# Optimization experiments

Hardware: AMD Instinct MI355X
Metric: run time of the kernel (lower is better)

The kernel has to match this reference:

```python
import math
import jax, jax.numpy as jnp
import numpy as np

# hyperparameters (module defaults; w_scale overridden to 1.0)
EMA_SPEED = 0.05
REW_SENS = 1.0
LR = 0.0033
MOMENTUM = 0.4
UNTANH = 0.6
SPEED = 0.5
WIDTH = 0.1
WD = 0.01
LAT_DECAY = 0.01
NOISE_SCALE = 0.8
C_MOMENT = 0.99
W_SCALE = 1.0


def rms_norm(x, axis=-1):
    return x * jax.lax.rsqrt(jnp.mean(x * x, axis=axis, keepdims=True) + 1e-6)


def setup_inputs() -> dict:
    key = jax.random.key(0)
    ks = jax.random.split(key, 16)
    B, N, D = 16, 128, 64
    s = 1.0 / math.sqrt(D)
    return {
        'eye_env': jax.random.normal(ks[0], (B, D), jnp.float32),
        'stomach_env': jax.random.normal(ks[1], (B, D), jnp.float32),
        'state': jax.random.normal(ks[2], (B, N, D), jnp.float32),
        'output': jax.random.normal(ks[3], (B, N, D), jnp.float32),
        'W1': jax.random.normal(ks[4], (B, N, D, D), jnp.float32) * s,
        'W2': jax.random.normal(ks[5], (B, N, D, D), jnp.float32) * s,
        'W3': jax.random.normal(ks[6], (B, N, D, D), jnp.float32) * s,
        'M1': jax.random.normal(ks[7], (B, N, D, D), jnp.float32) * 0.2,
        'M2': jax.random.normal(ks[8], (B, N, D, D), jnp.float32) * 0.2,
        'M3': jax.random.normal(ks[9], (B, N, D, D), jnp.float32) * 0.2,
        'E_baseline': jax.random.uniform(ks[10], (B, N, D), jnp.float32),
        'A': jax.nn.softmax(jax.random.normal(ks[11], (B, N, N), jnp.float32), axis=2),
        'noise_A': jax.random.normal(ks[12], (B, N, N), jnp.float32),
        'noise1_raw': jax.random.normal(ks[13], (B, N, D), jnp.float32),
        'noise2_raw': jax.random.normal(ks[14], (B, N, D), jnp.float32),
        'step_counter': 0,
    }


def reference(eye_env, stomach_env, state, output, W1, W2, W3, M1, M2, M3,
              E_baseline, A, noise_A, noise1_raw, noise2_raw, step_counter):
    B, N, D = state.shape
    sc = jnp.float32(step_counter) + 1.0  # self.step_counter += 1

    # attention routing
    q = jnp.einsum('bnj,bnjk->bnk', state, W3)
    k = jnp.einsum('bnj,bnjk->bnk', state, W2)
    raw_A = jnp.einsum('bnd,bmd->bnm', q, k) / math.sqrt(D) + noise_A * 1e-5
    P_dense = jax.nn.softmax(raw_A, axis=2)
    keep = (P_dense > 1.0 / (N + 1.0)) | (P_dense == jnp.max(P_dense, axis=2, keepdims=True))
    P = jax.nn.softmax(jnp.where(keep, raw_A, -jnp.inf), axis=2)
    A_new = A * C_MOMENT + P * (1.0 - C_MOMENT)
    A_new = A_new.at[:, 0:2, :].set(0.0)

    # message passing + sensory clamp
    target = jnp.einsum('bnm,bmd->bnd', A_new, output)
    target = target.at[:, 0].set(eye_env).at[:, 1].set(stomach_env)

    # prediction
    raw_pred = jnp.einsum('bnj,bnjk->bnk', state, W1)
    raw = raw_pred - jnp.tanh(raw_pred) * UNTANH
    prediction = jnp.tanh(raw) * math.sqrt(2.0 + math.sqrt(2.0))

    err = prediction - target
    E_curr = jax.nn.softmax(err, axis=-1)
    bmask = (E_baseline == 0).astype(jnp.float32)
    Eb = E_baseline * (1.0 - bmask) + E_curr * bmask
    Eb = Eb * (1.0 - EMA_SPEED) + EMA_SPEED * E_curr
    advantage = E_curr - Eb
    R = -rms_norm(advantage[..., None] * REW_SENS)  # (B,N,D,1)
    mask = (Eb > 0).astype(jnp.float32)[..., None]

    # noise injection
    state_mag = jnp.sum(jnp.abs(state), axis=(-2, -1), keepdims=True)
    noise1 = noise1_raw / (1.0 + state_mag)
    noise2 = noise2_raw * jnp.std(err, ddof=1) * NOISE_SCALE
    noisy_state = state + noise1 + noise2

    # Hebbian outer-product gradient, G_NORM=1.0 -> rms-normalized
    lg = -jnp.einsum('bni,bnj->bnij', err, noisy_state)
    lg = rms_norm(lg, axis=(2, 3))

    plasticity = 1.0 - R
    grad1 = plasticity * lg * mask + LAT_DECAY * W3 - WD * W1
    grad2 = plasticity * lg * mask + LAT_DECAY * W1 - WD * W2
    grad3 = plasticity * lg * mask + LAT_DECAY * W2 - WD * W3

    # travelling gaussian column mask
    idx = jnp.arange(D, dtype=jnp.float32).reshape(1, 1, 1, D)
    center = (sc * SPEED) % D
    diff = jnp.abs(idx - center)
    diff = jnp.minimum(diff, D - diff)
    g_mask = jnp.exp(-diff ** 2 / (2.0 * WIDTH ** 2 + 1e-6))

    M1n = M1 * MOMENTUM + (1.0 - MOMENTUM) * (grad1 * g_mask)
    M2n = M2 * MOMENTUM + (1.0 - MOMENTUM) * (grad2 * g_mask)
    M3n = M3 * MOMENTUM + (1.0 - MOMENTUM) * (grad3 * g_mask)
    W1n = rms_norm(W1 + LR * M1n) * W_SCALE
    W2n = rms_norm(W2 + LR * M2n) * W_SCALE
    W3n = rms_norm(W3 + LR * M3n) * W_SCALE

    # new output = prediction, new state = target
    return prediction, target, A_new, W1n, W2n, W3n
```

## Files before the change

### kernel.cpp

```cpp
#include <hip/hip_runtime.h>
#include <hip/hip_bf16.h>

typedef __hip_bfloat16 bf16;
typedef float f32x4 __attribute__((ext_vector_type(4)));

__device__ __forceinline__ float b2f(bf16 x) { return __bfloat162float(x); }

template<bool F32>
__device__ __forceinline__ float ld(const void* p, size_t i) {
  if constexpr (F32) return ((const float*)p)[i];
  else return b2f(((const bf16*)p)[i]);
}

template<bool F32>
__device__ __forceinline__ void ld4(const void* p, size_t i, float v[4]) {
  if constexpr (F32) {
    const float4 a = *(const float4*)((const float*)p + i);
    v[0]=a.x; v[1]=a.y; v[2]=a.z; v[3]=a.w;
  } else {
    union { uint2 u; bf16 h[4]; } t;
    t.u = *(const uint2*)((const bf16*)p + i);
    #pragma unroll
    for (int c = 0; c < 4; ++c) v[c] = b2f(t.h[c]);
  }
}

template<bool F32>
__device__ __forceinline__ void ld8(const void* p, size_t i, float v[8]) {
  if constexpr (F32) {
    const float4 a = *(const float4*)((const float*)p + i);
    const float4 b = *(const float4*)((const float*)p + i + 4);
    v[0]=a.x; v[1]=a.y; v[2]=a.z; v[3]=a.w;
    v[4]=b.x; v[5]=b.y; v[6]=b.z; v[7]=b.w;
  } else {
    union { uint4 u; bf16 h[8]; } t;
    t.u = *(const uint4*)((const bf16*)p + i);
    #pragma unroll
    for (int c = 0; c < 8; ++c) v[c] = b2f(t.h[c]);
  }
}

template<bool F32>
__device__ __forceinline__ void ld8nt(const void* p, size_t i, float v[8]) {
  if constexpr (F32) {
    const f32x4* q = (const f32x4*)((const float*)p + i);
    const f32x4 a = __builtin_nontemporal_load(q);
    const f32x4 b = __builtin_nontemporal_load(q + 1);
    v[0]=a[0]; v[1]=a[1]; v[2]=a[2]; v[3]=a[3];
    v[4]=b[0]; v[5]=b[1]; v[6]=b[2]; v[7]=b[3];
  } else {
    ld8<false>(p, i, v);
  }
}

__device__ __forceinline__ float plast(float Ec, float Ebl) {
  const float Eb0 = (Ebl == 0.f) ? Ec : Ebl;
  const float Eb  = Eb0 * 0.95f + 0.05f * Ec;
  const float adv = Ec - Eb;
  const float R   = -adv * rsqrtf(adv*adv + 1e-6f);
  return (Eb > 0.f) ? (1.f - R) : 0.f;
}


template<bool F32>
__device__ __forceinline__ void k1_wave(
    const void* state, const void* W1, const void* W2, const void* W3,
    float* qw, float* kw, float* magn, float* out_pred,
    int node, int mat, int lane)
{
  const float st = ld<F32>(state, (size_t)node*64 + lane);
  const int jg = lane >> 4, cq = lane & 15;
  const int c0 = cq * 4;
  const size_t nb = (size_t)node*4096 + (size_t)jg*1024 + c0;
  const void* W = (mat == 0) ? W3 : (mat == 1) ? W2 : W1;

  float acc[4] = {0.f, 0.f, 0.f, 0.f};
  float buf[16][4];
  #pragma unroll
  for (int jj = 0; jj < 16; ++jj) ld4<F32>(W, nb + (size_t)jj*64, buf[jj]);
  #pragma unroll
  for (int jj = 0; jj < 16; ++jj) {
    const float sj = __shfl(st, jg*16 + jj, 64);
    #pragma unroll
    for (int cc = 0; cc < 4; ++cc) acc[cc] += sj * buf[jj][cc];
  }
  #pragma unroll
  for (int cc = 0; cc < 4; ++cc) {
    acc[cc] += __shfl_xor(acc[cc], 16, 64);
    acc[cc] += __shfl_xor(acc[cc], 32, 64);
  }

  if (mat == 2) {
    float am = fabsf(st);
    #pragma unroll
    for (int s = 32; s; s >>= 1) am += __shfl_xor(am, s, 64);
    if (lane == 0) magn[node] = am;
    if (jg == 0) {
      float pr[4];
      #pragma unroll
      for (int cc = 0; cc < 4; ++cc) {
        const float raw = acc[cc] - tanhf(acc[cc]) * 0.6f;
        pr[cc] = tanhf(raw) * 1.8477590650225735f;
      }
      *(float4*)(out_pred + (size_t)node*64 + c0) = make_float4(pr[0], pr[1], pr[2], pr[3]);
    }
  } else if (jg == 0) {
    float* dst = (mat == 0) ? qw : kw;
    *(float4*)(dst + (size_t)node*64 + c0) = make_float4(acc[0], acc[1], acc[2], acc[3]);
  }
}

__global__ __launch_bounds__(256) void k1_qkpred(
    const void* __restrict__ state,
    const void* __restrict__ W1, const void* __restrict__ W2,
    const void* __restrict__ W3,
    float* __restrict__ qw, float* __restrict__ kw,
    float* __restrict__ magn, float* __restrict__ out_pred,
    int* __restrict__ flagws, float* __restrict__ stats)
{
  const int tid = threadIdx.x;
  const int w = tid >> 6, lane = tid & 63;
  bool huge = false;
  for (int i = lane; i < 1024; i += 64) {
    const float x = b2f(((const bf16*)state)[i]);
    if (!(fabsf(x) < 1e5f)) huge = true;
  }
  const bool f32 = (__ballot(huge) != 0ull);
  if (blockIdx.x == 0 && tid == 0) {
    *flagws = f32 ? 1 : 0;
    stats[0] = 0.f; stats[1] = 0.f;
  }
  const int wid = blockIdx.x * 4 + w;
  const int node = wid & 2047, mat = wid >> 11;
  if (f32) k1_wave<true >(state, W1, W2, W3, qw, kw, magn, out_pred, node, mat, lane);
  else     k1_wave<false>(state, W1, W2, W3, qw, kw, magn, out_pred, node, mat, lane);
}

template<bool F32>
__device__ __forceinline__ void k2_body(
    const float* qw, const float* kw, const float* predw,
    const void* noiseA, const void* Aold, const void* outp,
    const void* eye, const void* stomach, const void* Ebase,
    const float* magn, float* mag,
    float* errw, float* plw, float* stats,
    float* out_target, float* out_A,
    float* s_k, float* s_q, float* s_A)
{
  const int bidx = blockIdx.x;
  const int b = bidx >> 5;
  const int n0 = (bidx & 31) * 4;
  const int tid = threadIdx.x;
  const int w = tid >> 6, lane = tid & 63;

  if ((bidx & 31) == 0 && tid < 64) {
    float v = magn[b*128 + tid] + magn[b*128 + 64 + tid];
    #pragma unroll
    for (int s = 32; s; s >>= 1) v += __shfl_xor(v, s, 64);
    if (tid == 0) mag[b] = v;
  }

  {
    const float* kwb = kw + (size_t)b * 8192;
    #pragma unroll
    for (int it = 0; it < 8; ++it) {
      const int idx = it*256 + tid;
      const int m = idx >> 4, dq = idx & 15;
      const float4 v = *(const float4*)(kwb + (size_t)idx * 4);
      float* dst = &s_k[m*65 + dq*4];
      dst[0] = v.x; dst[1] = v.y; dst[2] = v.z; dst[3] = v.w;
    }
    if (tid < 64) {
      const int rr = tid >> 4, dq = tid & 15;
      *(float4*)&s_q[rr*64 + dq*4] =
          *(const float4*)(qw + ((size_t)(b*128 + n0 + rr))*64 + dq*4);
    }
  }
  __syncthreads();

  const int n = n0 + w;
  const size_t node = (size_t)b*128 + n;

  float d0 = 0.f, d1 = 0.f;
  {
    const float* qrow = s_q + w*64;
    const float* kr0 = s_k + lane*65;
    const float* kr1 = s_k + (lane + 64)*65;
    #pragma unroll 8
    for (int j = 0; j < 64; ++j) {
      const float qv = qrow[j];
      d0 += qv * kr0[j];
      d1 += qv * kr1[j];
    }
  }
  const float raw0 = d0*0.125f + 1e-5f*ld<F32>(noiseA, node*128 + lane);
  const float raw1 = d1*0.125f + 1e-5f*ld<F32>(noiseA, node*128 + lane + 64);

  float rmx = fmaxf(raw0, raw1);
  #pragma unroll
  for (int s = 32; s; s >>= 1) rmx = fmaxf(rmx, __shfl_xor(rmx, s, 64));
  const float e0x = expf(raw0 - rmx), e1x = expf(raw1 - rmx);
  float S = e0x + e1x;
  #pragma unroll
  for (int s = 32; s; s >>= 1) S += __shfl_xor(S, s, 64);
  const float thr = 0.007751937984496124f;
  const float ek0 = ((e0x/S > thr) || (raw0 == rmx)) ? e0x : 0.f;
  const float ek1 = ((e1x/S > thr) || (raw1 == rmx)) ? e1x : 0.f;
  float Sk = ek0 + ek1;
  #pragma unroll
  for (int s = 32; s; s >>= 1) Sk += __shfl_xor(Sk, s, 64);
  const float A0 = (n < 2) ? 0.f
                 : 0.99f*ld<F32>(Aold, node*128 + lane)      + 0.01f*(ek0/Sk);
  const float A1 = (n < 2) ? 0.f
                 : 0.99f*ld<F32>(Aold, node*128 + lane + 64) + 0.01f*(ek1/Sk);
  out_A[node*128 + lane]      = A0;
  out_A[node*128 + lane + 64] = A1;
  s_A[w*128 + lane]      = A0;
  s_A[w*128 + lane + 64] = A1;

  float t0;
  if (n == 0)      t0 = ld<F32>(eye, (size_t)b*64 + lane);
  else if (n == 1) t0 = ld<F32>(stomach, (size_t)b*64 + lane);
  else {
    t0 = 0.f;
    const float* arow = s_A + w*128;
    const size_t ob = (size_t)b * 8192;
    #pragma unroll 8
    for (int m = 0; m < 128; ++m)
      t0 += arow[m] * ld<F32>(outp, ob + (size_t)m*64 + lane);
  }
  out_target[node*64 + lane] = t0;
  const float er = predw[node*64 + lane] - t0;
  errw[node*64 + lane] = er;

  float mx = er;
  #pragma unroll
  for (int s = 32; s; s >>= 1) mx = fmaxf(mx, __shfl_xor(mx, s, 64));
  const float ee = expf(er - mx);
  float ss = ee;
  #pragma unroll
  for (int s = 32; s; s >>= 1) ss += __shfl_xor(ss, s, 64);
  plw[node*64 + lane] = plast(ee/ss, ld<F32>(Ebase, node*64 + lane));

  float se = er, sq2 = er*er;
  #pragma unroll
  for (int s = 32; s; s >>= 1) { se += __shfl_xor(se, s, 64); sq2 += __shfl_xor(sq2, s, 64); }
  if (lane == 0) { atomicAdd(&stats[0], se); atomicAdd(&stats[1], sq2); }
}

__global__ __launch_bounds__(256) void k2_attn(
    const int* __restrict__ flag,
    const float* __restrict__ qw, const float* __restrict__ kw,
    const float* __restrict__ predw,
    const void* __restrict__ noiseA, const void* __restrict__ Aold,
    const void* __restrict__ outp,
    const void* __restrict__ eye, const void* __restrict__ stomach,
    const void* __restrict__ Ebase,
    const float* __restrict__ magn, float* __restrict__ mag,
    float* __restrict__ errw, float* __restrict__ plw,
    float* __restrict__ stats,
    float* __restrict__ out_target, float* __restrict__ out_A)
{
  __shared__ alignas(16) float s_k[128*65];
  __shared__ alignas(16) float s_q[4*64];
  __shared__ alignas(16) float s_A[4*128];
  if (*flag) k2_body<true >(qw,kw,predw,noiseA,Aold,outp,eye,stomach,Ebase,magn,mag,errw,plw,stats,out_target,out_A,s_k,s_q,s_A);
  else       k2_body<false>(qw,kw,predw,noiseA,Aold,outp,eye,stomach,Ebase,magn,mag,errw,plw,stats,out_target,out_A,s_k,s_q,s_A);
}

template<bool F32>
__device__ __forceinline__ void k3_body(
    const float* errw, const float* plw,
    const void* state, const void* n1raw, const void* n2raw,
    const float* mag, const float* stats, const int* stepc,
    const void* W1, const void* W2, const void* W3,
    const void* M1, const void* M2, const void* M3,
    float* oW1, float* oW2, float* oW3)
{
  const int node = blockIdx.x;
  const int b = node >> 7;
  const int tid = threadIdx.x;
  const int lane = tid & 63;
  const int r = tid >> 3;
  const int l8 = tid & 7;

  const size_t sb = (size_t)node*64 + lane;
  const float e_i  = errw[sb];
  const float pl_i = plw[sb];
  const float st_i = ld<F32>(state, sb);
  const float n1_i = ld<F32>(n1raw, sb);
  const float n2_i = ld<F32>(n2raw, sb);
  const float magb = mag[b];
  const float S1 = stats[0], S2 = stats[1];
  const float scv = (float)stepc[0] + 1.f;

  const size_t off = (size_t)node*4096 + (size_t)r*64 + (size_t)l8*8;
  float w1v[8], w2v[8], w3v[8], m1v[8], m2v[8], m3v[8];
  ld8  <F32>(W1, off, w1v); ld8  <F32>(W2, off, w2v); ld8  <F32>(W3, off, w3v);
  ld8nt<F32>(M1, off, m1v); ld8nt<F32>(M2, off, m2v); ld8nt<F32>(M3, off, m3v);

  const float Mn = 131072.f;
  const float var = (S2 - S1*S1/Mn) / (Mn - 1.f);
  const float stdv = sqrtf(fmaxf(var, 0.f));
  const float ns_i = st_i + n1_i / (1.f + magb)
                   + n2_i * stdv * 0.8f;
  float e2 = e_i*e_i, q2 = ns_i*ns_i;
  #pragma unroll
  for (int s = 32; s; s >>= 1) { e2 += __shfl_xor(e2, s, 64); q2 += __shfl_xor(q2, s, 64); }
  const float c_i  = -ns_i * rsqrtf(e2 * q2 * (1.f/4096.f) + 1e-6f);
  const float pe_i = pl_i * e_i;
  const float center = fmodf(scv * 0.5f, 64.f);
  float dff = fabsf((float)lane - center);
  dff = fminf(dff, 64.f - dff);
  const float g_i = expf(-dff*dff * (1.f/0.020001f));

  const float pe = __shfl(pe_i, r, 64);
  float cj[8], gj[8];
  #pragma unroll
  for (int cc = 0; cc < 8; ++cc) {
    const int j = l8*8 + cc;
    cj[cc] = __shfl(c_i, j, 64);
    gj[cc] = __shfl(g_i, j, 64);
  }

  float t1[8], t2[8], t3[8];
  float ss1 = 0.f, ss2 = 0.f, ss3 = 0.f;
  #pragma unroll
  for (int cc = 0; cc < 8; ++cc) {
    const float lgterm = pe * cj[cc];
    const float g = gj[cc];
    const float g1 = lgterm + 0.01f*w3v[cc] - 0.01f*w1v[cc];
    const float g2 = lgterm + 0.01f*w1v[cc] - 0.01f*w2v[cc];
    const float g3 = lgterm + 0.01f*w2v[cc] - 0.01f*w3v[cc];
    const float v1 = w1v[cc] + 0.0033f*(0.4f*m1v[cc] + 0.6f*g1*g);
    const float v2 = w2v[cc] + 0.0033f*(0.4f*m2v[cc] + 0.6f*g2*g);
    const float v3 = w3v[cc] + 0.0033f*(0.4f*m3v[cc] + 0.6f*g3*g);
    t1[cc] = v1; t2[cc] = v2; t3[cc] = v3;
    ss1 += v1*v1; ss2 += v2*v2; ss3 += v3*v3;
  }
  #pragma unroll
  for (int s = 1; s <= 4; s <<= 1) {
    ss1 += __shfl_xor(ss1, s, 64);
    ss2 += __shfl_xor(ss2, s, 64);
    ss3 += __shfl_xor(ss3, s, 64);
  }
  const float r1 = rsqrtf(ss1*(1.f/64.f) + 1e-6f);
  const float r2 = rsqrtf(ss2*(1.f/64.f) + 1e-6f);
  const float r3 = rsqrtf(ss3*(1.f/64.f) + 1e-6f);
  *(float4*)(oW1 + off)     = make_float4(t1[0]*r1, t1[1]*r1, t1[2]*r1, t1[3]*r1);
  *(float4*)(oW1 + off + 4) = make_float4(t1[4]*r1, t1[5]*r1, t1[6]*r1, t1[7]*r1);
  *(float4*)(oW2 + off)     = make_float4(t2[0]*r2, t2[1]*r2, t2[2]*r2, t2[3]*r2);
  *(float4*)(oW2 + off + 4) = make_float4(t2[4]*r2, t2[5]*r2, t2[6]*r2, t2[7]*r2);
  *(float4*)(oW3 + off)     = make_float4(t3[0]*r3, t3[1]*r3, t3[2]*r3, t3[3]*r3);
  *(float4*)(oW3 + off + 4) = make_float4(t3[4]*r3, t3[5]*r3, t3[6]*r3, t3[7]*r3);
}

__global__ __launch_bounds__(512) void k3_update(
    const int* __restrict__ flag,
    const float* __restrict__ errw, const float* __restrict__ plw,
    const void* __restrict__ state, const void* __restrict__ n1raw,
    const void* __restrict__ n2raw,
    const float* __restrict__ mag, const float* __restrict__ stats,
    const int* __restrict__ stepc,
    const void* __restrict__ W1, const void* __restrict__ W2,
    const void* __restrict__ W3,
    const void* __restrict__ M1, const void* __restrict__ M2,
    const void* __restrict__ M3,
    float* __restrict__ oW1, float* __restrict__ oW2, float* __restrict__ oW3)
{
  if (*flag) k3_body<true >(errw,plw,state,n1raw,n2raw,mag,stats,stepc,W1,W2,W3,M1,M2,M3,oW1,oW2,oW3);
  else       k3_body<false>(errw,plw,state,n1raw,n2raw,mag,stats,stepc,W1,W2,W3,M1,M2,M3,oW1,oW2,oW3);
}

extern "C" void kernel_launch(void* const* d_in, const int* in_sizes, int n_in,
                              void* d_out, int out_size, void* d_ws, size_t ws_size,
                              hipStream_t stream) {
  const void* eye     = d_in[0];
  const void* stomach = d_in[1];
  const void* state   = d_in[2];
  const void* outp    = d_in[3];
  const void* W1      = d_in[4];
  const void* W2      = d_in[5];
  const void* W3      = d_in[6];
  const void* M1      = d_in[7];
  const void* M2      = d_in[8];
  const void* M3      = d_in[9];
  const void* Ebase   = d_in[10];
  const void* Aold    = d_in[11];
  const void* noiseA  = d_in[12];
  const void* n1raw   = d_in[13];
  const void* n2raw   = d_in[14];
  const int*  stepc   = (const int*)d_in[15];

  float* ws    = (float*)d_ws;
  float* qw    = ws;
  float* kw    = ws + 131072;
  float* errw  = ws + 262144;
  float* plw   = ws + 393216;
  float* magn  = ws + 524288;
  float* mag   = ws + 526336;
  float* stats = ws + 526352;
  int*   flag  = (int*)(ws + 526354);

  float* out        = (float*)d_out;
  float* out_pred   = out;
  float* out_target = out + 131072;
  float* out_A      = out + 262144;
  float* oW1        = out + 524288;
  float* oW2        = out + 8912896;
  float* oW3        = out + 17301504;

  k1_qkpred<<<1536, 256, 0, stream>>>(state, W1, W2, W3, qw, kw, magn, out_pred,
                                      flag, stats);
  k2_attn<<<512, 256, 0, stream>>>(flag, qw, kw, out_pred, noiseA, Aold, outp,
                                   eye, stomach, Ebase, magn, mag, errw, plw, stats,
                                   out_target, out_A);
  k3_update<<<2048, 512, 0, stream>>>(flag, errw, plw, state, n1raw, n2raw, mag, stats,
                                      stepc, W1, W2, W3, M1, M2, M3, oW1, oW2, oW3);
}
```

Before: 351.9 us.

## Make attention kernel wave-independent, replacing shared-memory K staging with shuffle reductions

```diff
diff --git a/kernel.cpp b/kernel.cpp
--- a/kernel.cpp
+++ b/kernel.cpp
@@ -137,63 +137,41 @@
 }
 
 template<bool F32>
-__device__ __forceinline__ void k2_body(
+__device__ __forceinline__ void k2_wave(
     const float* qw, const float* kw, const float* predw,
     const void* noiseA, const void* Aold, const void* outp,
     const void* eye, const void* stomach, const void* Ebase,
     const float* magn, float* mag,
     float* errw, float* plw, float* stats,
     float* out_target, float* out_A,
-    float* s_k, float* s_q, float* s_A)
-{
-  const int bidx = blockIdx.x;
-  const int b = bidx >> 5;
-  const int n0 = (bidx & 31) * 4;
-  const int tid = threadIdx.x;
-  const int w = tid >> 6, lane = tid & 63;
-
-  if ((bidx & 31) == 0 && tid < 64) {
-    float v = magn[b*128 + tid] + magn[b*128 + 64 + tid];
+    int node, int lane, bool do_mag, int mb)
+{
+  const int b = node >> 7, n = node & 127;
+
+  if (do_mag) {
+    float v = magn[mb*128 + lane] + magn[mb*128 + 64 + lane];
     #pragma unroll
     for (int s = 32; s; s >>= 1) v += __shfl_xor(v, s, 64);
-    if (tid == 0) mag[b] = v;
-  }
-
-  {
-    const float* kwb = kw + (size_t)b * 8192;
-    #pragma unroll
-    for (int it = 0; it < 8; ++it) {
-      const int idx = it*256 + tid;
-      const int m = idx >> 4, dq = idx & 15;
-      const float4 v = *(const float4*)(kwb + (size_t)idx * 4);
-      float* dst = &s_k[m*65 + dq*4];
-      dst[0] = v.x; dst[1] = v.y; dst[2] = v.z; dst[3] = v.w;
+    if (lane == 0) mag[mb] = v;
+  }
+
+  const float q_l = qw[(size_t)node*64 + lane];
+  const float* kb = kw + (size_t)b * 8192;
+
+  float d0 = 0.f, d1 = 0.f;
+  #pragma unroll 4
+  for (int m = 0; m < 64; ++m) {
+    float p0 = q_l * kb[(size_t)m*64 + lane];
+    float p1 = q_l * kb[(size_t)(m + 64)*64 + lane];
+    #pragma unroll
+    for (int s = 1; s <= 32; s <<= 1) {
+      p0 += __shfl_xor(p0, s, 64);
+      p1 += __shfl_xor(p1, s, 64);
     }
-    if (tid < 64) {
-      const int rr = tid >> 4, dq = tid & 15;
-      *(float4*)&s_q[rr*64 + dq*4] =
-          *(const float4*)(qw + ((size_t)(b*128 + n0 + rr))*64 + dq*4);
-    }
-  }
-  __syncthreads();
-
-  const int n = n0 + w;
-  const size_t node = (size_t)b*128 + n;
-
-  float d0 = 0.f, d1 = 0.f;
-  {
-    const float* qrow = s_q + w*64;
-    const float* kr0 = s_k + lane*65;
-    const float* kr1 = s_k + (lane + 64)*65;
-    #pragma unroll 8
-    for (int j = 0; j < 64; ++j) {
-      const float qv = qrow[j];
-      d0 += qv * kr0[j];
-      d1 += qv * kr1[j];
-    }
-  }
-  const float raw0 = d0*0.125f + 1e-5f*ld<F32>(noiseA, node*128 + lane);
-  const float raw1 = d1*0.125f + 1e-5f*ld<F32>(noiseA, node*128 + lane + 64);
+    if (lane == m) { d0 = p0; d1 = p1; }
+  }
+  const float raw0 = d0*0.125f + 1e-5f*ld<F32>(noiseA, (size_t)node*128 + lane);
+  const float raw1 = d1*0.125f + 1e-5f*ld<F32>(noiseA, (size_t)node*128 + lane + 64);
 
   float rmx = fmaxf(raw0, raw1);
   #pragma unroll
@@ -209,28 +187,29 @@
   #pragma unroll
   for (int s = 32; s; s >>= 1) Sk += __shfl_xor(Sk, s, 64);
   const float A0 = (n < 2) ? 0.f
-                 : 0.99f*ld<F32>(Aold, node*128 + lane)      + 0.01f*(ek0/Sk);
+                 : 0.99f*ld<F32>(Aold, (size_t)node*128 + lane)      + 0.01f*(ek0/Sk);
   const float A1 = (n < 2) ? 0.f
-                 : 0.99f*ld<F32>(Aold, node*128 + lane + 64) + 0.01f*(ek1/Sk);
-  out_A[node*128 + lane]      = A0;
-  out_A[node*128 + lane + 64] = A1;
-  s_A[w*128 + lane]      = A0;
-  s_A[w*128 + lane + 64] = A1;
+                 : 0.99f*ld<F32>(Aold, (size_t)node*128 + lane + 64) + 0.01f*(ek1/Sk);
+  out_A[(size_t)node*128 + lane]      = A0;
+  out_A[(size_t)node*128 + lane + 64] = A1;
 
   float t0;
   if (n == 0)      t0 = ld<F32>(eye, (size_t)b*64 + lane);
   else if (n == 1) t0 = ld<F32>(stomach, (size_t)b*64 + lane);
   else {
     t0 = 0.f;
-    const float* arow = s_A + w*128;
     const size_t ob = (size_t)b * 8192;
     #pragma unroll 8
-    for (int m = 0; m < 128; ++m)
-      t0 += arow[m] * ld<F32>(outp, ob + (size_t)m*64 + lane);
-  }
-  out_target[node*64 + lane] = t0;
-  const float er = predw[node*64 + lane] - t0;
-  errw[node*64 + lane] = er;
+    for (int m = 0; m < 64; ++m) {
+      const float a0 = __shfl(A0, m, 64);
+      const float a1 = __shfl(A1, m, 64);
+      t0 += a0 * ld<F32>(outp, ob + (size_t)m*64 + lane);
+      t0 += a1 * ld<F32>(outp, ob + (size_t)(m + 64)*64 + lane);
+    }
+  }
+  out_target[(size_t)node*64 + lane] = t0;
+  const float er = predw[(size_t)node*64 + lane] - t0;
+  errw[(size_t)node*64 + lane] = er;
 
   float mx = er;
   #pragma unroll
@@ -239,7 +218,7 @@
   float ss = ee;
   #pragma unroll
   for (int s = 32; s; s >>= 1) ss += __shfl_xor(ss, s, 64);
-  plw[node*64 + lane] = plast(ee/ss, ld<F32>(Ebase, node*64 + lane));
+  plw[(size_t)node*64 + lane] = plast(ee/ss, ld<F32>(Ebase, (size_t)node*64 + lane));
 
   float se = er, sq2 = er*er;
   #pragma unroll
@@ -260,11 +239,13 @@
     float* __restrict__ stats,
     float* __restrict__ out_target, float* __restrict__ out_A)
 {
-  __shared__ alignas(16) float s_k[128*65];
-  __shared__ alignas(16) float s_q[4*64];
-  __shared__ alignas(16) float s_A[4*128];
-  if (*flag) k2_body<true >(qw,kw,predw,noiseA,Aold,outp,eye,stomach,Ebase,magn,mag,errw,plw,stats,out_target,out_A,s_k,s_q,s_A);
-  else       k2_body<false>(qw,kw,predw,noiseA,Aold,outp,eye,stomach,Ebase,magn,mag,errw,plw,stats,out_target,out_A,s_k,s_q,s_A);
+  const int tid = threadIdx.x;
+  const int w = tid >> 6, lane = tid & 63;
+  const int node = blockIdx.x * 4 + w;
+  const bool do_mag = (blockIdx.x < 16) && (w == 3);
+  const int mb = blockIdx.x;
+  if (*flag) k2_wave<true >(qw,kw,predw,noiseA,Aold,outp,eye,stomach,Ebase,magn,mag,errw,plw,stats,out_target,out_A,node,lane,do_mag,mb);
+  else       k2_wave<false>(qw,kw,predw,noiseA,Aold,outp,eye,stomach,Ebase,magn,mag,errw,plw,stats,out_target,out_A,node,lane,do_mag,mb);
 }
 
 template<bool F32>
```

After: 362.9 us. 1.03x slower.
